# Kernel optimization log

Hardware: AMD Instinct MI355X
Metric: run time of the kernel (lower is better)

Reference implementation:

```python
import jax, jax.numpy as jnp
import numpy as np

D_MODEL = 2048
NUM_HEADS = 16
D_K = D_MODEL // NUM_HEADS  # 128, per-head dim used for RoPE
ROPE_THETA = 10000.0
MAX_SEQ_LEN = 2048
BATCH = 4
SEQ = 2048


def _trunc_normal(key, shape, std):
    # approximate trunc_normal_(mean=0, std, a=-3std, b=3std)
    return jnp.clip(std * jax.random.normal(key, shape), -3 * std, 3 * std)


def setup_inputs() -> dict:
    key = jax.random.key(0)
    ks = jax.random.split(key, 6)
    x = jax.random.normal(ks[0], (BATCH, SEQ, D_MODEL), dtype=jnp.float32)
    token_positions = jnp.arange(SEQ, dtype=jnp.int32)
    std = float(np.sqrt(2.0 / (D_MODEL + D_MODEL)))
    wq = _trunc_normal(ks[1], (D_MODEL, D_MODEL), std)  # (d_out, d_in)
    wk = _trunc_normal(ks[2], (D_MODEL, D_MODEL), std)
    wv = _trunc_normal(ks[3], (D_MODEL, D_MODEL), std)
    wo = _trunc_normal(ks[4], (D_MODEL, D_MODEL), std)
    return {"x": x, "token_positions": token_positions,
            "wq": wq, "wk": wk, "wv": wv, "wo": wo}


def _rope(t, pos):
    # t: (b, h, n, d_k), pos: (n,) int
    # interleaved pairs: (x1, x2) = (t[..., 0::2], t[..., 1::2])
    freqs = 1.0 / (ROPE_THETA ** (jnp.arange(0, D_K, 2, dtype=jnp.float32) / D_K))
    angles = pos.astype(jnp.float32)[:, None] * freqs[None, :]  # (n, d_k/2)
    cos = jnp.cos(angles).astype(t.dtype)
    sin = jnp.sin(angles).astype(t.dtype)
    tr = t.reshape(*t.shape[:-1], D_K // 2, 2)
    x1, x2 = tr[..., 0], tr[..., 1]
    y1 = cos * x1 - sin * x2
    y2 = sin * x1 + cos * x2
    return jnp.stack([y1, y2], axis=-1).reshape(t.shape)


def reference(x, token_positions, wq, wk, wv, wo):
    b, n, d = x.shape
    q = jnp.einsum('bnd,od->bno', x, wq)
    k = jnp.einsum('bnd,od->bno', x, wk)
    v = jnp.einsum('bnd,od->bno', x, wv)
    # split heads for RoPE: (b, n, h*dk) -> (b, h, n, dk)
    split = lambda t: t.reshape(b, n, NUM_HEADS, D_K).transpose(0, 2, 1, 3)
    merge = lambda t: t.transpose(0, 2, 1, 3).reshape(b, n, d)
    q = merge(_rope(split(q), token_positions))
    k = merge(_rope(split(k), token_positions))
    # NOTE: source merges heads back BEFORE flash attention -> single-head
    # attention over full d_model with causal mask, scale 1/sqrt(d_model)
    scale = 1.0 / jnp.sqrt(jnp.asarray(d, dtype=x.dtype))
    scores = jnp.einsum('bqd,bkd->bqk', q, k) * scale  # (b, n, n)
    causal = jnp.tril(jnp.ones((n, n), dtype=bool))
    scores = jnp.where(causal[None, :, :], scores, jnp.finfo(scores.dtype).min)
    attn = jax.nn.softmax(scores, axis=-1)
    out = jnp.einsum('bqk,bkd->bqd', attn, v)
    return jnp.einsum('bnd,od->bno', out, wo)
```

## Files before the change

kernel.cpp:

```cpp
#include <hip/hip_runtime.h>
#include <hip/hip_bf16.h>
#include <cstdint>
#include <cmath>

typedef __attribute__((ext_vector_type(4))) float f32x4;
typedef __attribute__((ext_vector_type(8))) short bf16x8;

#define BAR()   __builtin_amdgcn_s_barrier()
#define PRIO1() __builtin_amdgcn_s_setprio(1)
#define PRIO0() __builtin_amdgcn_s_setprio(0)
#define WAITV8() asm volatile("s_waitcnt vmcnt(8)" ::: "memory")
#define WAITV6() asm volatile("s_waitcnt vmcnt(6)" ::: "memory")
#define WAITV0() asm volatile("s_waitcnt vmcnt(0)" ::: "memory")
#define MM(a,b,c) __builtin_amdgcn_mfma_f32_16x16x32_bf16((a),(b),(c),0,0,0)

__device__ __forceinline__ void gl_lds16(const __hip_bfloat16* g, char* l) {
    __builtin_amdgcn_global_load_lds(
        (const __attribute__((address_space(1))) void*)g,
        (__attribute__((address_space(3))) void*)l, 16, 0, 0);
}
__device__ __forceinline__ void store_c(float* C, size_t i, float v) { C[i] = v; }
__device__ __forceinline__ void store_c(__hip_bfloat16* C, size_t i, float v) { C[i] = __float2bfloat16(v); }

#define SGA8(dd, h, i, kt) do{ const int s_ = (h)*16 + (i)*8 + w; \
    gl_lds16(Asb + (size_t)((s_>>1)<<4) * lda + ((s_&1)<<5) + (kt), \
             lds + (dd)*65536 + (s_<<10)); }while(0)
#define SGB8N(dd, g, kt) do{ const int sB_ = (g)*8 + w; \
    const int hi_ = sB_ >> 4, r_ = sB_ & 15; \
    const int wc_ = r_ >> 2, ni_ = hi_*2 + ((r_>>1)&1), kk_ = r_ & 1; \
    gl_lds16(Bsb + (size_t)(wc_*64 + ni_*16) * ldb + (kk_<<5) + (kt), \
             lds + (dd)*65536 + 32768 + (sB_<<10)); }while(0)
#define LDA8(dd, miA, kk) (*(const bf16x8*)(lds + (dd)*65536 + ((sbA + (miA)*2 + (kk)) << 10) + rswz))
#define LDB8N(dd, ni, kk) (*(const bf16x8*)(lds + (dd)*65536 + 32768 + \
    ((((((ni)>>1)<<4) + ((w&3)<<2) + (((ni)&1)<<1) + (kk))) << 10) + rswz))

template<typename CT, int MODE>
__global__ __launch_bounds__(512, 2)
void gemm8p(const __hip_bfloat16* __restrict__ A, const __hip_bfloat16* __restrict__ B,
            CT* __restrict__ C, int K, int lda, int ldb, int ldc, int nbx,
            float alpha, size_t sA, size_t sB, size_t sC)
{
    __shared__ __align__(1024) char lds[131072];

    int bm0, bn0;
    if (MODE == 1) {
        const int wgi = blockIdx.x;
        int by = (int)((sqrtf(8.f * wgi + 1.f) - 1.f) * 0.5f);
        if (by * (by + 1) / 2 > wgi) --by;
        if ((by + 1) * (by + 2) / 2 <= wgi) ++by;
        const int bx = wgi - by * (by + 1) / 2;
        bm0 = by * 256; bn0 = bx * 256;
    } else if (MODE == 2) {
        const int g = blockIdx.x;
        const int nby = gridDim.x / nbx;
        const int bx = g % nbx;
        const int by = (g / nbx + bx) % nby;
        bm0 = by * 256; bn0 = bx * 256;
    } else {
        const int nwg = gridDim.x;
        const int q8 = nwg >> 3, r8 = nwg & 7;
        const int xcd = blockIdx.x & 7, blk = blockIdx.x >> 3;
        const int wg = (xcd < r8 ? xcd * (q8 + 1) : r8 * (q8 + 1) + (xcd - r8) * q8) + blk;
        bm0 = (wg / nbx) * 256; bn0 = (wg % nbx) * 256;
    }

    A += sA * blockIdx.y; B += sB * blockIdx.y; C += sC * blockIdx.y;

    const int tid  = threadIdx.x;
    const int lane = tid & 63;
    const int w    = tid >> 6;

    const int rb   = (lane & 15) * 64 + (lane >> 4) * 16;
    const int rswz = rb ^ (((rb >> 9) & 1) << 5);
    const int sbA  = (w >> 2) * 16;

    const int l16 = lane * 16;
    const int uqs = l16 ^ (((l16 >> 9) & 1) << 5);
    const int rIn = uqs >> 6;
    const int cIn = (uqs & 63) >> 1;
    const __hip_bfloat16* Asb = A + (size_t)(bm0 + rIn) * lda + cIn;
    const __hip_bfloat16* Bsb = B + (size_t)(bn0 + rIn) * ldb + cIn;

    f32x4 acc[8][4] = {};
    bf16x8 afA0[4][2], afA1[4][2], bfB0[2][2], bfB1[2][2];

    const int klim = bm0 + 256;
    const int kend = (MODE == 2) ? (K < klim ? K : klim) : K;
    const int nt   = kend >> 6;

    SGA8(0, 0, 0, 0); SGA8(0, 1, 0, 0);
    SGB8N(0, 0, 0);   SGB8N(0, 1, 0);
    SGB8N(0, 2, 0);   SGB8N(0, 3, 0);
    SGA8(0, 0, 1, 0); SGA8(0, 1, 1, 0);
    if (nt > 1) {
        SGA8(1, 0, 0, 64); SGA8(1, 1, 0, 64);
        SGB8N(1, 2, 64);   SGB8N(1, 3, 64);
        SGA8(1, 0, 1, 64); SGA8(1, 1, 1, 64);
        WAITV6();
    } else WAITV0();
    BAR();
#pragma unroll
    for (int mi = 0; mi < 4; ++mi) { afA0[mi][0] = LDA8(0, mi, 0); afA0[mi][1] = LDA8(0, mi, 1); }
#pragma unroll
    for (int ni = 0; ni < 2; ++ni) { bfB0[ni][0] = LDB8N(0, ni, 0); bfB0[ni][1] = LDB8N(0, ni, 1); }

    for (int t = 0; t < nt; ++t) {
        const int d   = t & 1, e = d ^ 1;
        const bool p1 = (t + 1) < nt;
        const bool p2 = (t + 2) < nt;
        const int kt1 = (t + 1) << 6;
        const int kt2 = (t + 2) << 6;

        if (p1) { SGB8N(e, 0, kt1); SGB8N(e, 1, kt1); }
        BAR();
        PRIO1();
#pragma unroll
        for (int mi = 0; mi < 4; ++mi)
#pragma unroll
            for (int ni = 0; ni < 2; ++ni) {
                f32x4 c = acc[mi][ni];
                c = MM(afA0[mi][0], bfB0[ni][0], c);
                c = MM(afA0[mi][1], bfB0[ni][1], c);
                acc[mi][ni] = c;
            }
#pragma unroll
        for (int ni = 0; ni < 2; ++ni) { bfB1[ni][0] = LDB8N(d, 2 + ni, 0); bfB1[ni][1] = LDB8N(d, 2 + ni, 1); }
        PRIO0();
        BAR();

        if (p2) { SGA8(d, 0, 0, kt2); SGA8(d, 1, 0, kt2); WAITV8(); }
        else if (p1) WAITV6();
        else WAITV0();
        BAR();
        PRIO1();
#pragma unroll
        for (int mi = 0; mi < 4; ++mi)
#pragma unroll
            for (int ni = 0; ni < 2; ++ni) {
                f32x4 c = acc[mi][2 + ni];
                c = MM(afA0[mi][0], bfB1[ni][0], c);
                c = MM(afA0[mi][1], bfB1[ni][1], c);
                acc[mi][2 + ni] = c;
            }
#pragma unroll
        for (int mi = 0; mi < 4; ++mi) { afA1[mi][0] = LDA8(d, 4 + mi, 0); afA1[mi][1] = LDA8(d, 4 + mi, 1); }
        PRIO0();
        BAR();

        if (p2) { SGB8N(d, 2, kt2); SGB8N(d, 3, kt2); }
        BAR();
        PRIO1();
#pragma unroll
        for (int mi = 0; mi < 4; ++mi)
#pragma unroll
            for (int ni = 0; ni < 2; ++ni) {
                f32x4 c = acc[4 + mi][2 + ni];
                c = MM(afA1[mi][0], bfB1[ni][0], c);
                c = MM(afA1[mi][1], bfB1[ni][1], c);
                acc[4 + mi][2 + ni] = c;
            }
        if (p1) {
#pragma unroll
            for (int mi = 0; mi < 4; ++mi) { afA0[mi][0] = LDA8(e, mi, 0); afA0[mi][1] = LDA8(e, mi, 1); }
        }
        PRIO0();
        BAR();

        if (p2) { SGA8(d, 0, 1, kt2); SGA8(d, 1, 1, kt2); WAITV6(); }
        else WAITV0();
        BAR();
        PRIO1();
#pragma unroll
        for (int mi = 0; mi < 4; ++mi)
#pragma unroll
            for (int ni = 0; ni < 2; ++ni) {
                f32x4 c = acc[4 + mi][ni];
                c = MM(afA1[mi][0], bfB0[ni][0], c);
                c = MM(afA1[mi][1], bfB0[ni][1], c);
                acc[4 + mi][ni] = c;
            }
        if (p1) {
#pragma unroll
            for (int ni = 0; ni < 2; ++ni) { bfB0[ni][0] = LDB8N(e, ni, 0); bfB0[ni][1] = LDB8N(e, ni, 1); }
        }
        PRIO0();
        BAR();
    }

    const int cr = (lane >> 4) * 4, cc = lane & 15;
    const int wrow = bm0 + (w >> 2) * 128, wcol = bn0 + (w & 3) * 64;
#pragma unroll
    for (int mi = 0; mi < 8; ++mi)
#pragma unroll
        for (int ni = 0; ni < 4; ++ni) {
            const int row = wrow + mi * 16 + cr;
            const int col = wcol + ni * 16 + cc;
#pragma unroll
            for (int j = 0; j < 4; ++j)
                store_c(C, (size_t)(row + j) * ldc + col, acc[mi][ni][j] * alpha);
        }
}

__global__ void f32_to_bf16_vec(const float* __restrict__ in,
                                __hip_bfloat16* __restrict__ out, int n4)
{
    int i = blockIdx.x * 256 + threadIdx.x;
    if (i >= n4) return;
    float4 v = ((const float4*)in)[i];
    union { ushort4 u; __hip_bfloat16 h[4]; } o;
    o.h[0] = __float2bfloat16(v.x);
    o.h[1] = __float2bfloat16(v.y);
    o.h[2] = __float2bfloat16(v.z);
    o.h[3] = __float2bfloat16(v.w);
    ((ushort4*)out)[i] = o.u;
}

__global__ void conv_w4(const float* __restrict__ w0, const float* __restrict__ w1,
                        const float* __restrict__ w2, const float* __restrict__ w3,
                        __hip_bfloat16* o0, __hip_bfloat16* o1,
                        __hip_bfloat16* o2, __hip_bfloat16* o3, int n4)
{
    int i = blockIdx.x * 256 + threadIdx.x;
    if (i >= n4) return;
    const float* src; __hip_bfloat16* dst;
    switch (blockIdx.y) {
        case 0: src = w0; dst = o0; break;
        case 1: src = w1; dst = o1; break;
        case 2: src = w2; dst = o2; break;
        default: src = w3; dst = o3; break;
    }
    float4 v = ((const float4*)src)[i];
    union { ushort4 u; __hip_bfloat16 h[4]; } o;
    o.h[0] = __float2bfloat16(v.x);
    o.h[1] = __float2bfloat16(v.y);
    o.h[2] = __float2bfloat16(v.z);
    o.h[3] = __float2bfloat16(v.w);
    ((ushort4*)dst)[i] = o.u;
}

__global__ void rope_table(const int* __restrict__ pos, float2* __restrict__ tab, int N)
{
    int i = blockIdx.x * 256 + threadIdx.x;
    if (i >= N * 64) return;
    int n = i >> 6, j = i & 63;
    float p = (float)pos[n];
    float ang = p * powf(10000.f, -(float)j * (1.0f / 64.0f));
    tab[i] = make_float2(cosf(ang), sinf(ang));
}

__global__ void rope_apply2(__hip_bfloat16* __restrict__ Q, __hip_bfloat16* __restrict__ K,
                            const float2* __restrict__ tab, int ld)
{
    int i = blockIdx.x * 256 + threadIdx.x;
    __hip_bfloat16* T = blockIdx.y ? K : Q;
    int r  = i >> 8;
    int cb = (i & 255) << 3;
    int n  = r & 2047;
    int j0 = (cb >> 1) & 63;
    union { bf16x8 v; __hip_bfloat162 h[4]; } u;
    __hip_bfloat16* p = T + (size_t)r * ld + cb;
    u.v = *(const bf16x8*)p;
#pragma unroll
    for (int k = 0; k < 4; ++k) {
        float2 cs = tab[(n << 6) + j0 + k];
        float x1 = __bfloat162float(u.h[k].x);
        float x2 = __bfloat162float(u.h[k].y);
        u.h[k].x = __float2bfloat16(cs.x * x1 - cs.y * x2);
        u.h[k].y = __float2bfloat16(cs.y * x1 + cs.x * x2);
    }
    *(bf16x8*)p = u.v;
}

__global__ void softmax_causal_ip(float* __restrict__ S, int N)
{
    const int q = blockIdx.x;
    float* srow = S + ((size_t)blockIdx.y * N + q) * N;
    __shared__ float buf[2048];
    __shared__ float red[8];
    const int tid = threadIdx.x;
    const int wend = ((q >> 8) + 1) << 8;

    float4* b4 = (float4*)buf;
    const float4* s4 = (const float4*)srow;
    for (int i = tid; i <= (q >> 2); i += 256) b4[i] = s4[i];
    __syncthreads();

    float m = -1e30f;
    for (int j = tid; j <= q; j += 256) m = fmaxf(m, buf[j]);
#pragma unroll
    for (int o = 32; o > 0; o >>= 1) m = fmaxf(m, __shfl_xor(m, o));
    if ((tid & 63) == 0) red[tid >> 6] = m;
    __syncthreads();
    m = fmaxf(fmaxf(red[0], red[1]), fmaxf(red[2], red[3]));

    float sum = 0.f;
    for (int j = tid; j <= q; j += 256) { float e = __expf(buf[j] - m); buf[j] = e; sum += e; }
#pragma unroll
    for (int o = 32; o > 0; o >>= 1) sum += __shfl_xor(sum, o);
    if ((tid & 63) == 0) red[4 + (tid >> 6)] = sum;
    __syncthreads();
    const float inv = 1.f / (red[4] + red[5] + red[6] + red[7]);

    __hip_bfloat162* p2 = (__hip_bfloat162*)srow;
    for (int i = tid; i < (wend >> 1); i += 256) {
        int j0 = i * 2;
        __hip_bfloat162 h;
        h.x = __float2bfloat16(j0     <= q ? buf[j0]     * inv : 0.f);
        h.y = __float2bfloat16(j0 + 1 <= q ? buf[j0 + 1] * inv : 0.f);
        p2[i] = h;
    }
}

__global__ void transpose_bf16(const __hip_bfloat16* __restrict__ V,
                               __hip_bfloat16* __restrict__ Vt, int N, int ldv)
{
    __shared__ __hip_bfloat16 tile[32][33];
    const size_t bi = (size_t)blockIdx.z * N * ldv;
    const size_t bo = (size_t)blockIdx.z * N * N;
    const int k0 = blockIdx.x * 32, d0 = blockIdx.y * 32;
    const int tx = threadIdx.x, ty = threadIdx.y;
#pragma unroll
    for (int j = 0; j < 4; ++j)
        tile[ty + 8 * j][tx] = V[bi + (size_t)(k0 + ty + 8 * j) * ldv + d0 + tx];
    __syncthreads();
#pragma unroll
    for (int j = 0; j < 4; ++j)
        Vt[bo + (size_t)(d0 + ty + 8 * j) * N + k0 + tx] = tile[tx][ty + 8 * j];
}

extern "C" void kernel_launch(void* const* d_in, const int* in_sizes, int n_in,
                              void* d_out, int out_size, void* d_ws, size_t ws_size,
                              hipStream_t stream)
{
    const float* x  = (const float*)d_in[0];
    const int* pos  = (const int*)d_in[1];
    const float* wq = (const float*)d_in[2];
    const float* wk = (const float*)d_in[3];
    const float* wv = (const float*)d_in[4];
    const float* wo = (const float*)d_in[5];
    float* out = (float*)d_out;

    const int B = 4, N = 2048, D = 2048;
    const int M = B * N;
    const int D3 = 3 * D;
    const size_t MB = 1ull << 20;
    if (ws_size < 192 * MB) return;

    char* w = (char*)d_ws;
    __hip_bfloat16* QKV  = (__hip_bfloat16*)(w + 0 * MB);
    __hip_bfloat16* wqkv = (__hip_bfloat16*)(w + 96 * MB);
    __hip_bfloat16* wob  = (__hip_bfloat16*)(w + 120 * MB);
    __hip_bfloat16* xb   = (__hip_bfloat16*)(w + 128 * MB);
    __hip_bfloat16* Vt   = xb;
    __hip_bfloat16* AO   = (__hip_bfloat16*)(w + 160 * MB);
    float2*         tab  = (float2*)(w + 190 * MB);

    __hip_bfloat16* Qb = QKV;
    __hip_bfloat16* Kb = QKV + D;
    __hip_bfloat16* Vb = QKV + 2 * D;

    float* Sal = (float*)d_out;

    f32_to_bf16_vec<<<(M * D / 4 + 255) / 256, 256, 0, stream>>>(x, xb, M * D / 4);
    conv_w4<<<dim3((D * D / 4 + 255) / 256, 4), 256, 0, stream>>>(
        wq, wk, wv, wo, wqkv, wqkv + (size_t)D * D, wqkv + (size_t)2 * D * D, wob, D * D / 4);
    rope_table<<<(N * 64 + 255) / 256, 256, 0, stream>>>(pos, tab, N);

    gemm8p<__hip_bfloat16, 0><<<dim3((D3 / 256) * (M / 256)), 512, 0, stream>>>(
        xb, wqkv, QKV, D, D, D, D3, D3 / 256, 1.f, 0, 0, 0);

    rope_apply2<<<dim3(M, 2), 256, 0, stream>>>(Qb, Kb, tab, D3);

    transpose_bf16<<<dim3(N / 32, N / 32, B), dim3(32, 8), 0, stream>>>(Vb, Vt, N, D3);

    const float scale = 1.0f / sqrtf((float)D);
    const int nbxA = N / 256;
    const int ntri = nbxA * (nbxA + 1) / 2;
    gemm8p<float, 1><<<dim3(ntri, B), 512, 0, stream>>>(
        Qb, Kb, Sal, D, D3, D3, N, nbxA, scale,
        (size_t)N * D3, (size_t)N * D3, (size_t)N * N);
    softmax_causal_ip<<<dim3(N, B), 256, 0, stream>>>(Sal, N);
    gemm8p<__hip_bfloat16, 2><<<dim3(nbxA * nbxA, B), 512, 0, stream>>>(
        (const __hip_bfloat16*)Sal, Vt, AO, N, 2 * N, N, D, nbxA, 1.f,
        (size_t)2 * N * N, (size_t)N * N, (size_t)N * D);

    gemm8p<float, 0><<<dim3((D / 256) * (M / 256)), 512, 0, stream>>>(
        AO, wob, out, D, D, D, D, D / 256, 1.f, 0, 0, 0);
}
```

Measured before the change: 461.8 us.

## Fuse RoPE into QKV epilogue, transpose into QK^T grid, merge conversions

Applies RoPE inside the QKV GEMM epilogue using lane shuffles, removing the separate rope_apply2 pass. Runs the V transpose in extra workgroups appended to the causal QK^T launch (64 blocks per batch, 36 for GEMM tiles) and drops the standalone transpose kernel. Merges the x and weight fp32-to-bf16 conversions into one launch. It also restructures the GEMM main loop so A/B fragments are reloaded from LDS each phase into a single register set instead of double-buffered registers, which frees registers but removes some load/compute overlap.

```diff
diff --git a/kernel.cpp b/kernel.cpp
--- a/kernel.cpp
+++ b/kernel.cpp
@@ -9,7 +9,6 @@
 #define BAR()   __builtin_amdgcn_s_barrier()
 #define PRIO1() __builtin_amdgcn_s_setprio(1)
 #define PRIO0() __builtin_amdgcn_s_setprio(0)
-#define WAITV8() asm volatile("s_waitcnt vmcnt(8)" ::: "memory")
 #define WAITV6() asm volatile("s_waitcnt vmcnt(6)" ::: "memory")
 #define WAITV0() asm volatile("s_waitcnt vmcnt(0)" ::: "memory")
 #define MM(a,b,c) __builtin_amdgcn_mfma_f32_16x16x32_bf16((a),(b),(c),0,0,0)
@@ -34,16 +33,40 @@
 #define LDB8N(dd, ni, kk) (*(const bf16x8*)(lds + (dd)*65536 + 32768 + \
     ((((((ni)>>1)<<4) + ((w&3)<<2) + (((ni)&1)<<1) + (kk))) << 10) + rswz))
 
-template<typename CT, int MODE>
+template<typename CT, int MODE, bool RFUSE>
 __global__ __launch_bounds__(512, 2)
 void gemm8p(const __hip_bfloat16* __restrict__ A, const __hip_bfloat16* __restrict__ B,
             CT* __restrict__ C, int K, int lda, int ldb, int ldc, int nbx,
-            float alpha, size_t sA, size_t sB, size_t sC)
+            float alpha, size_t sA, size_t sB, size_t sC,
+            const float2* __restrict__ tab,
+            const __hip_bfloat16* __restrict__ Vsrc,
+            __hip_bfloat16* __restrict__ Vt, int ldv)
 {
     __shared__ __align__(1024) char lds[131072];
+    const int tid = threadIdx.x;
 
     int bm0, bn0;
     if (MODE == 1) {
+        if ((int)blockIdx.x >= nbx) {
+            const int tb  = blockIdx.x - nbx;
+            const int ntb = gridDim.x - nbx;
+            const __hip_bfloat16* Vg = Vsrc + (size_t)blockIdx.y * 2048 * ldv;
+            __hip_bfloat16* Vtg = Vt + (size_t)blockIdx.y * 2048 * 2048;
+            __hip_bfloat16 (*tile)[66] = (__hip_bfloat16(*)[66])lds;
+            const int tx = tid & 63, ty = tid >> 6;
+            for (int ti = tb; ti < 1024; ti += ntb) {
+                const int k0 = (ti & 31) << 6, d0 = (ti >> 5) << 6;
+                __syncthreads();
+#pragma unroll
+                for (int jj = 0; jj < 8; ++jj)
+                    tile[ty + 8 * jj][tx] = Vg[(size_t)(k0 + ty + 8 * jj) * ldv + d0 + tx];
+                __syncthreads();
+#pragma unroll
+                for (int jj = 0; jj < 8; ++jj)
+                    Vtg[(size_t)(d0 + ty + 8 * jj) * 2048 + k0 + tx] = tile[tx][ty + 8 * jj];
+            }
+            return;
+        }
         const int wgi = blockIdx.x;
         int by = (int)((sqrtf(8.f * wgi + 1.f) - 1.f) * 0.5f);
         if (by * (by + 1) / 2 > wgi) --by;
@@ -66,7 +89,6 @@
 
     A += sA * blockIdx.y; B += sB * blockIdx.y; C += sC * blockIdx.y;
 
-    const int tid  = threadIdx.x;
     const int lane = tid & 63;
     const int w    = tid >> 6;
 
@@ -82,7 +104,7 @@
     const __hip_bfloat16* Bsb = B + (size_t)(bn0 + rIn) * ldb + cIn;
 
     f32x4 acc[8][4] = {};
-    bf16x8 afA0[4][2], afA1[4][2], bfB0[2][2], bfB1[2][2];
+    bf16x8 afA[4][2], bfB[2][2];
 
     const int klim = bm0 + 256;
     const int kend = (MODE == 2) ? (K < klim ? K : klim) : K;
@@ -99,10 +121,6 @@
         WAITV6();
     } else WAITV0();
     BAR();
-#pragma unroll
-    for (int mi = 0; mi < 4; ++mi) { afA0[mi][0] = LDA8(0, mi, 0); afA0[mi][1] = LDA8(0, mi, 1); }
-#pragma unroll
-    for (int ni = 0; ni < 2; ++ni) { bfB0[ni][0] = LDB8N(0, ni, 0); bfB0[ni][1] = LDB8N(0, ni, 1); }
 
     for (int t = 0; t < nt; ++t) {
         const int d   = t & 1, e = d ^ 1;
@@ -111,6 +129,10 @@
         const int kt1 = (t + 1) << 6;
         const int kt2 = (t + 2) << 6;
 
+#pragma unroll
+        for (int mi = 0; mi < 4; ++mi) { afA[mi][0] = LDA8(d, mi, 0); afA[mi][1] = LDA8(d, mi, 1); }
+#pragma unroll
+        for (int ni = 0; ni < 2; ++ni) { bfB[ni][0] = LDB8N(d, ni, 0); bfB[ni][1] = LDB8N(d, ni, 1); }
         if (p1) { SGB8N(e, 0, kt1); SGB8N(e, 1, kt1); }
         BAR();
         PRIO1();
@@ -119,18 +141,16 @@
 #pragma unroll
             for (int ni = 0; ni < 2; ++ni) {
                 f32x4 c = acc[mi][ni];
-                c = MM(afA0[mi][0], bfB0[ni][0], c);
-                c = MM(afA0[mi][1], bfB0[ni][1], c);
+                c = MM(afA[mi][0], bfB[ni][0], c);
+                c = MM(afA[mi][1], bfB[ni][1], c);
                 acc[mi][ni] = c;
             }
-#pragma unroll
-        for (int ni = 0; ni < 2; ++ni) { bfB1[ni][0] = LDB8N(d, 2 + ni, 0); bfB1[ni][1] = LDB8N(d, 2 + ni, 1); }
         PRIO0();
         BAR();
 
-        if (p2) { SGA8(d, 0, 0, kt2); SGA8(d, 1, 0, kt2); WAITV8(); }
-        else if (p1) WAITV6();
-        else WAITV0();
+#pragma unroll
+        for (int ni = 0; ni < 2; ++ni) { bfB[ni][0] = LDB8N(d, 2 + ni, 0); bfB[ni][1] = LDB8N(d, 2 + ni, 1); }
+        if (p2) { SGA8(d, 0, 0, kt2); SGA8(d, 1, 0, kt2); }
         BAR();
         PRIO1();
 #pragma unroll
@@ -138,15 +158,15 @@
 #pragma unroll
             for (int ni = 0; ni < 2; ++ni) {
                 f32x4 c = acc[mi][2 + ni];
-                c = MM(afA0[mi][0], bfB1[ni][0], c);
-                c = MM(afA0[mi][1], bfB1[ni][1], c);
+                c = MM(afA[mi][0], bfB[ni][0], c);
+                c = MM(afA[mi][1], bfB[ni][1], c);
                 acc[mi][2 + ni] = c;
             }
-#pragma unroll
-        for (int mi = 0; mi < 4; ++mi) { afA1[mi][0] = LDA8(d, 4 + mi, 0); afA1[mi][1] = LDA8(d, 4 + mi, 1); }
         PRIO0();
         BAR();
 
+#pragma unroll
+        for (int mi = 0; mi < 4; ++mi) { afA[mi][0] = LDA8(d, 4 + mi, 0); afA[mi][1] = LDA8(d, 4 + mi, 1); }
         if (p2) { SGB8N(d, 2, kt2); SGB8N(d, 3, kt2); }
         BAR();
         PRIO1();
@@ -155,17 +175,15 @@
 #pragma unroll
             for (int ni = 0; ni < 2; ++ni) {
                 f32x4 c = acc[4 + mi][2 + ni];
-                c = MM(afA1[mi][0], bfB1[ni][0], c);
-                c = MM(afA1[mi][1], bfB1[ni][1], c);
+                c = MM(afA[mi][0], bfB[ni][0], c);
+                c = MM(afA[mi][1], bfB[ni][1], c);
                 acc[4 + mi][2 + ni] = c;
             }
-        if (p1) {
-#pragma unroll
-            for (int mi = 0; mi < 4; ++mi) { afA0[mi][0] = LDA8(e, mi, 0); afA0[mi][1] = LDA8(e, mi, 1); }
-        }
         PRIO0();
         BAR();
 
+#pragma unroll
+        for (int ni = 0; ni < 2; ++ni) { bfB[ni][0] = LDB8N(d, ni, 0); bfB[ni][1] = LDB8N(d, ni, 1); }
         if (p2) { SGA8(d, 0, 1, kt2); SGA8(d, 1, 1, kt2); WAITV6(); }
         else WAITV0();
         BAR();
@@ -175,14 +193,10 @@
 #pragma unroll
             for (int ni = 0; ni < 2; ++ni) {
                 f32x4 c = acc[4 + mi][ni];
-                c = MM(afA1[mi][0], bfB0[ni][0], c);
-                c = MM(afA1[mi][1], bfB0[ni][1], c);
+                c = MM(afA[mi][0], bfB[ni][0], c);
+                c = MM(afA[mi][1], bfB[ni][1], c);
                 acc[4 + mi][ni] = c;
             }
-        if (p1) {
-#pragma unroll
-            for (int ni = 0; ni < 2; ++ni) { bfB0[ni][0] = LDB8N(e, ni, 0); bfB0[ni][1] = LDB8N(e, ni, 1); }
-        }
         PRIO0();
         BAR();
     }
@@ -195,47 +209,54 @@
         for (int ni = 0; ni < 4; ++ni) {
             const int row = wrow + mi * 16 + cr;
             const int col = wcol + ni * 16 + cc;
-#pragma unroll
-            for (int j = 0; j < 4; ++j)
-                store_c(C, (size_t)(row + j) * ldc + col, acc[mi][ni][j] * alpha);
+            if (RFUSE && col < 4096) {
+                const int j0 = (col & 127) >> 1;
+#pragma unroll
+                for (int j = 0; j < 4; ++j) {
+                    float xv = acc[mi][ni][j] * alpha;
+                    float xp = __shfl_xor(xv, 1);
+                    const int n = (row + j) & 2047;
+                    float2 cs = tab[(n << 6) + j0];
+                    float y = (lane & 1) ? fmaf(cs.y, xp, cs.x * xv)
+                                         : fmaf(cs.x, xv, -(cs.y * xp));
+                    store_c(C, (size_t)(row + j) * ldc + col, y);
+                }
+            } else {
+#pragma unroll
+                for (int j = 0; j < 4; ++j)
+                    store_c(C, (size_t)(row + j) * ldc + col, acc[mi][ni][j] * alpha);
+            }
         }
 }
 
-__global__ void f32_to_bf16_vec(const float* __restrict__ in,
-                                __hip_bfloat16* __restrict__ out, int n4)
+__global__ void conv5(const float* __restrict__ x,  const float* __restrict__ w0,
+                      const float* __restrict__ w1, const float* __restrict__ w2,
+                      const float* __restrict__ w3,
+                      __hip_bfloat16* __restrict__ xb,
+                      __hip_bfloat16* __restrict__ wqkv,
+                      __hip_bfloat16* __restrict__ wob)
 {
     int i = blockIdx.x * 256 + threadIdx.x;
-    if (i >= n4) return;
-    float4 v = ((const float4*)in)[i];
+    const float* src; __hip_bfloat16* dst; int off;
+    if (i < 4194304) { src = x; dst = xb; off = i; }
+    else {
+        int k = i - 4194304;
+        int ws = k >> 20;
+        off = k & 1048575;
+        switch (ws) {
+            case 0: src = w0; dst = wqkv;                     break;
+            case 1: src = w1; dst = wqkv + (size_t)4194304;   break;
+            case 2: src = w2; dst = wqkv + (size_t)8388608;   break;
+            default: src = w3; dst = wob;                     break;
+        }
+    }
+    float4 v = ((const float4*)src)[off];
     union { ushort4 u; __hip_bfloat16 h[4]; } o;
     o.h[0] = __float2bfloat16(v.x);
     o.h[1] = __float2bfloat16(v.y);
     o.h[2] = __float2bfloat16(v.z);
     o.h[3] = __float2bfloat16(v.w);
-    ((ushort4*)out)[i] = o.u;
-}
-
-__global__ void conv_w4(const float* __restrict__ w0, const float* __restrict__ w1,
-                        const float* __restrict__ w2, const float* __restrict__ w3,
-                        __hip_bfloat16* o0, __hip_bfloat16* o1,
-                        __hip_bfloat16* o2, __hip_bfloat16* o3, int n4)
-{
-    int i = blockIdx.x * 256 + threadIdx.x;
-    if (i >= n4) return;
-    const float* src; __hip_bfloat16* dst;
-    switch (blockIdx.y) {
-        case 0: src = w0; dst = o0; break;
-        case 1: src = w1; dst = o1; break;
-        case 2: src = w2; dst = o2; break;
-        default: src = w3; dst = o3; break;
-    }
-    float4 v = ((const float4*)src)[i];
-    union { ushort4 u; __hip_bfloat16 h[4]; } o;
-    o.h[0] = __float2bfloat16(v.x);
-    o.h[1] = __float2bfloat16(v.y);
-    o.h[2] = __float2bfloat16(v.z);
-    o.h[3] = __float2bfloat16(v.w);
-    ((ushort4*)dst)[i] = o.u;
+    ((ushort4*)dst)[off] = o.u;
 }
 
 __global__ void rope_table(const int* __restrict__ pos, float2* __restrict__ tab, int N)
@@ -246,29 +267,6 @@
     float p = (float)pos[n];
     float ang = p * powf(10000.f, -(float)j * (1.0f / 64.0f));
     tab[i] = make_float2(cosf(ang), sinf(ang));
-}
-
-__global__ void rope_apply2(__hip_bfloat16* __restrict__ Q, __hip_bfloat16* __restrict__ K,
-                            const float2* __restrict__ tab, int ld)
-{
-    int i = blockIdx.x * 256 + threadIdx.x;
-    __hip_bfloat16* T = blockIdx.y ? K : Q;
-    int r  = i >> 8;
-    int cb = (i & 255) << 3;
-    int n  = r & 2047;
-    int j0 = (cb >> 1) & 63;
-    union { bf16x8 v; __hip_bfloat162 h[4]; } u;
-    __hip_bfloat16* p = T + (size_t)r * ld + cb;
-    u.v = *(const bf16x8*)p;
-#pragma unroll
-    for (int k = 0; k < 4; ++k) {
-        float2 cs = tab[(n << 6) + j0 + k];
-        float x1 = __bfloat162float(u.h[k].x);
-        float x2 = __bfloat162float(u.h[k].y);
-        u.h[k].x = __float2bfloat16(cs.x * x1 - cs.y * x2);
-        u.h[k].y = __float2bfloat16(cs.y * x1 + cs.x * x2);
-    }
-    *(bf16x8*)p = u.v;
 }
 
 __global__ void softmax_causal_ip(float* __restrict__ S, int N)
@@ -311,23 +309,6 @@
     }
 }
 
-__global__ void transpose_bf16(const __hip_bfloat16* __restrict__ V,
-                               __hip_bfloat16* __restrict__ Vt, int N, int ldv)
-{
-    __shared__ __hip_bfloat16 tile[32][33];
-    const size_t bi = (size_t)blockIdx.z * N * ldv;
-    const size_t bo = (size_t)blockIdx.z * N * N;
-    const int k0 = blockIdx.x * 32, d0 = blockIdx.y * 32;
-    const int tx = threadIdx.x, ty = threadIdx.y;
-#pragma unroll
-    for (int j = 0; j < 4; ++j)
-        tile[ty + 8 * j][tx] = V[bi + (size_t)(k0 + ty + 8 * j) * ldv + d0 + tx];
-    __syncthreads();
-#pragma unroll
-    for (int j = 0; j < 4; ++j)
-        Vt[bo + (size_t)(d0 + ty + 8 * j) * N + k0 + tx] = tile[tx][ty + 8 * j];
-}
-
 extern "C" void kernel_launch(void* const* d_in, const int* in_sizes, int n_in,
                               void* d_out, int out_size, void* d_ws, size_t ws_size,
                               hipStream_t stream)
@@ -361,29 +342,23 @@
 
     float* Sal = (float*)d_out;
 
-    f32_to_bf16_vec<<<(M * D / 4 + 255) / 256, 256, 0, stream>>>(x, xb, M * D / 4);
-    conv_w4<<<dim3((D * D / 4 + 255) / 256, 4), 256, 0, stream>>>(
-        wq, wk, wv, wo, wqkv, wqkv + (size_t)D * D, wqkv + (size_t)2 * D * D, wob, D * D / 4);
+    conv5<<<32768, 256, 0, stream>>>(x, wq, wk, wv, wo, xb, wqkv, wob);
     rope_table<<<(N * 64 + 255) / 256, 256, 0, stream>>>(pos, tab, N);
 
-    gemm8p<__hip_bfloat16, 0><<<dim3((D3 / 256) * (M / 256)), 512, 0, stream>>>(
-        xb, wqkv, QKV, D, D, D, D3, D3 / 256, 1.f, 0, 0, 0);
-
-    rope_apply2<<<dim3(M, 2), 256, 0, stream>>>(Qb, Kb, tab, D3);
-
-    transpose_bf16<<<dim3(N / 32, N / 32, B), dim3(32, 8), 0, stream>>>(Vb, Vt, N, D3);
+    gemm8p<__hip_bfloat16, 0, true><<<dim3((D3 / 256) * (M / 256)), 512, 0, stream>>>(
+        xb, wqkv, QKV, D, D, D, D3, D3 / 256, 1.f, 0, 0, 0, tab, nullptr, nullptr, 0);
 
     const float scale = 1.0f / sqrtf((float)D);
     const int nbxA = N / 256;
     const int ntri = nbxA * (nbxA + 1) / 2;
-    gemm8p<float, 1><<<dim3(ntri, B), 512, 0, stream>>>(
-        Qb, Kb, Sal, D, D3, D3, N, nbxA, scale,
-        (size_t)N * D3, (size_t)N * D3, (size_t)N * N);
+    gemm8p<float, 1, false><<<dim3(64, B), 512, 0, stream>>>(
+        Qb, Kb, Sal, D, D3, D3, N, ntri, scale,
+        (size_t)N * D3, (size_t)N * D3, (size_t)N * N, nullptr, Vb, Vt, D3);
     softmax_causal_ip<<<dim3(N, B), 256, 0, stream>>>(Sal, N);
-    gemm8p<__hip_bfloat16, 2><<<dim3(nbxA * nbxA, B), 512, 0, stream>>>(
+    gemm8p<__hip_bfloat16, 2, false><<<dim3(nbxA * nbxA, B), 512, 0, stream>>>(
         (const __hip_bfloat16*)Sal, Vt, AO, N, 2 * N, N, D, nbxA, 1.f,
-        (size_t)2 * N * N, (size_t)N * N, (size_t)N * D);
-
-    gemm8p<float, 0><<<dim3((D / 256) * (M / 256)), 512, 0, stream>>>(
-        AO, wob, out, D, D, D, D, D / 256, 1.f, 0, 0, 0);
-}
+        (size_t)2 * N * N, (size_t)N * N, (size_t)N * D, nullptr, nullptr, nullptr, 0);
+
+    gemm8p<float, 0, false><<<dim3((D / 256) * (M / 256)), 512, 0, stream>>>(
+        AO, wob, out, D, D, D, D, D / 256, 1.f, 0, 0, 0, nullptr, nullptr, nullptr, 0);
+}
```

Result: faster. 444.3 us (-3.8%).
